# Optimization experiments

Hardware: AMD Instinct MI355X
Metric: run time of the kernel (lower is better)

## Reference

```python
import jax, jax.numpy as jnp
import numpy as np


def squash(s, axis=-1):
    sq = jnp.sum(s ** 2, axis=axis, keepdims=True)
    return sq / (1.0 + sq) * s / (jnp.sqrt(sq) + 1e-08)


def setup_inputs() -> dict:
    key = jax.random.key(0)
    B, C, H, W, D = 16, 64, 64, 64, 16
    inp = jax.random.normal(key, (B, C, H, W, D), dtype=jnp.float32)
    return {"inp": inp, "kernel_size": 2, "routing_iteration": 3}


def reference(inp, kernel_size, routing_iteration):
    B, C, H, W, D = inp.shape
    k = kernel_size
    nH, nW = H // k, W // k
    T = nH * nW
    kk = k * k
    # Extract non-overlapping k x k tiles (x-major, then y), flatten tile -> [B,C,T,kk,D]
    u = inp.reshape(B, C, nH, k, nW, k, D)
    u = u.transpose(0, 1, 2, 4, 3, 5, 6).reshape(B, C, T, kk, D)
    # u_hat gets a singleton "output capsule" axis (dim=1 in the original per-tile view)
    u_hat = u[:, :, :, None, :, :]            # [B,C,T,1,kk,D]
    temp_u_hat = jax.lax.stop_gradient(u_hat)  # detach
    b = jnp.zeros((B, C, T, 1, kk, 1), dtype=inp.dtype)
    for _ in range(routing_iteration - 1):
        c = jax.nn.softmax(b, axis=3)          # softmax over singleton axis -> ones (faithful)
        s = jnp.sum(c * temp_u_hat, axis=4)    # [B,C,T,1,D]
        v = squash(s)
        # uv = temp_u_hat @ v^T over D: [B,C,T,1,kk,1]
        uv = jnp.einsum('bctikd,bctid->bctik', temp_u_hat, v)[..., None]
        b = b + uv
    c = jax.nn.softmax(b, axis=3)
    s = jnp.sum(c * u_hat, axis=4)             # [B,C,T,1,D]
    v = squash(s)                              # [B,C,T,1,D]
    out = v[:, :, :, 0, :].reshape(B, C, nH, nW, D)
    return out
```

## Files before the change

### kernel.cpp

```cpp
#include <hip/hip_runtime.h>


#define B_  16
#define C_  64
#define H_  64
#define W_  64
#define D_  16
#define NH_ 32
#define NW_ 32
#define NVEC (B_ * C_ * NH_ * NW_)

typedef float f4 __attribute__((ext_vector_type(4)));

__global__ __launch_bounds__(256)
void caps_pool_squash_kernel(const float* __restrict__ in, float* __restrict__ out) {
    const unsigned stride = gridDim.x * 256u;
    const unsigned total  = NVEC * 4u;

    for (unsigned tid = blockIdx.x * 256u + threadIdx.x; tid < total; tid += stride) {
        const unsigned vec = tid >> 2;
        const unsigned q   = tid & 3u;

        const unsigned bc  = vec >> 10;
        const unsigned rem = vec & 1023u;
        const unsigned nh  = rem >> 5;
        const unsigned nw  = rem & 31u;

        const unsigned base = ((bc * H_ + 2u * nh) * W_ + 2u * nw) * D_ + q * 4u;

        const f4 a = __builtin_nontemporal_load((const f4*)(in + base));
        const f4 b = __builtin_nontemporal_load((const f4*)(in + base + D_));
        const f4 c = __builtin_nontemporal_load((const f4*)(in + base + W_ * D_));
        const f4 d = __builtin_nontemporal_load((const f4*)(in + base + W_ * D_ + D_));

        const f4 s = (a + b) + (c + d);

        float p = s.x * s.x + s.y * s.y + s.z * s.z + s.w * s.w;
        p += __shfl_xor(p, 1, 64);
        p += __shfl_xor(p, 2, 64);

        const float scale = p / ((1.0f + p) * (sqrtf(p) + 1e-8f));

        const f4 v = s * scale;
        __builtin_nontemporal_store(v, (f4*)(out + vec * (unsigned)D_ + q * 4u));
    }
}

extern "C" void kernel_launch(void* const* d_in, const int* in_sizes, int n_in,
                              void* d_out, int out_size, void* d_ws, size_t ws_size,
                              hipStream_t stream) {
    const float* inp = (const float*)d_in[0];
    float* out = (float*)d_out;

    caps_pool_squash_kernel<<<2048, 256, 0, stream>>>(inp, out);
}
```

Baseline: 62.55 us.

## Load contiguous rows per wave and pool 2x2 tiles via cross-lane shuffles

Each wavefront now handles 16 output capsules. It loads two full contiguous 1 KB input rows with one fully coalesced f4 per lane per segment, instead of four strided 64-byte pieces per capsule. The horizontal pair sum and the gather into output order are done with xor and indexed shuffles. The grid-stride loop is replaced by one launch covering all work exactly once, and the nontemporal load and store hints are dropped. This aims at better memory coalescing on a bandwidth-bound kernel, at the cost of extra shuffle instructions and possible cache pollution without the streaming hints.

```diff
diff --git a/kernel.cpp b/kernel.cpp
--- a/kernel.cpp
+++ b/kernel.cpp
@@ -6,44 +6,56 @@
 #define H_  64
 #define W_  64
 #define D_  16
-#define NH_ 32
-#define NW_ 32
-#define NVEC (B_ * C_ * NH_ * NW_)
+#define NVEC (B_ * C_ * 32 * 32)
 
 typedef float f4 __attribute__((ext_vector_type(4)));
 
 __global__ __launch_bounds__(256)
 void caps_pool_squash_kernel(const float* __restrict__ in, float* __restrict__ out) {
-    const unsigned stride = gridDim.x * 256u;
-    const unsigned total  = NVEC * 4u;
+    const unsigned tid  = blockIdx.x * 256u + threadIdx.x;
+    const unsigned wave = tid >> 6;
+    const unsigned lane = tid & 63u;
 
-    for (unsigned tid = blockIdx.x * 256u + threadIdx.x; tid < total; tid += stride) {
-        const unsigned vec = tid >> 2;
-        const unsigned q   = tid & 3u;
+    const unsigned bc  = wave >> 6;
+    const unsigned rem = (wave << 4) & 1023u;
+    const unsigned nh  = rem >> 5;
+    const unsigned nw0 = rem & 31u;
 
-        const unsigned bc  = vec >> 10;
-        const unsigned rem = vec & 1023u;
-        const unsigned nh  = rem >> 5;
-        const unsigned nw  = rem & 31u;
+    const unsigned ibase = bc * (H_ * W_ * D_) + (2u * nh) * (W_ * D_) + (2u * nw0) * D_;
 
-        const unsigned base = ((bc * H_ + 2u * nh) * W_ + 2u * nw) * D_ + q * 4u;
+    const f4 x0 = *(const f4*)(in + ibase + lane * 4u);
+    const f4 x1 = *(const f4*)(in + ibase + 256u + lane * 4u);
+    const f4 y0 = *(const f4*)(in + ibase + 1024u + lane * 4u);
+    const f4 y1 = *(const f4*)(in + ibase + 1280u + lane * 4u);
 
-        const f4 a = __builtin_nontemporal_load((const f4*)(in + base));
-        const f4 b = __builtin_nontemporal_load((const f4*)(in + base + D_));
-        const f4 c = __builtin_nontemporal_load((const f4*)(in + base + W_ * D_));
-        const f4 d = __builtin_nontemporal_load((const f4*)(in + base + W_ * D_ + D_));
+    f4 z0 = x0 + y0;
+    f4 z1 = x1 + y1;
 
-        const f4 s = (a + b) + (c + d);
+    z0.x += __shfl_xor(z0.x, 4, 64);  z0.y += __shfl_xor(z0.y, 4, 64);
+    z0.z += __shfl_xor(z0.z, 4, 64);  z0.w += __shfl_xor(z0.w, 4, 64);
+    z1.x += __shfl_xor(z1.x, 4, 64);  z1.y += __shfl_xor(z1.y, 4, 64);
+    z1.z += __shfl_xor(z1.z, 4, 64);  z1.w += __shfl_xor(z1.w, 4, 64);
 
-        float p = s.x * s.x + s.y * s.y + s.z * s.z + s.w * s.w;
-        p += __shfl_xor(p, 1, 64);
-        p += __shfl_xor(p, 2, 64);
+    const int src = (int)(((lane >> 2) & 7u) * 8u + (lane & 3u));
+    f4 s;
+    {
+        const float a0 = __shfl(z0.x, src, 64), b0 = __shfl(z1.x, src, 64);
+        const float a1 = __shfl(z0.y, src, 64), b1 = __shfl(z1.y, src, 64);
+        const float a2 = __shfl(z0.z, src, 64), b2 = __shfl(z1.z, src, 64);
+        const float a3 = __shfl(z0.w, src, 64), b3 = __shfl(z1.w, src, 64);
+        const bool lo = lane < 32u;
+        s.x = lo ? a0 : b0;  s.y = lo ? a1 : b1;
+        s.z = lo ? a2 : b2;  s.w = lo ? a3 : b3;
+    }
 
-        const float scale = p / ((1.0f + p) * (sqrtf(p) + 1e-8f));
+    float p = s.x * s.x + s.y * s.y + s.z * s.z + s.w * s.w;
+    p += __shfl_xor(p, 1, 64);
+    p += __shfl_xor(p, 2, 64);
+    const float scale = p / ((1.0f + p) * (sqrtf(p) + 1e-8f));
 
-        const f4 v = s * scale;
-        __builtin_nontemporal_store(v, (f4*)(out + vec * (unsigned)D_ + q * 4u));
-    }
+    const f4 v = s * scale;
+
+    *(f4*)(out + wave * 256u + lane * 4u) = v;
 }
 
 extern "C" void kernel_launch(void* const* d_in, const int* in_sizes, int n_in,
@@ -52,5 +64,7 @@
     const float* inp = (const float*)d_in[0];
     float* out = (float*)d_out;
 
-    caps_pool_squash_kernel<<<2048, 256, 0, stream>>>(inp, out);
+    const unsigned waves  = NVEC / 16u;
+    const unsigned blocks = (waves * 64u) / 256u;
+    caps_pool_squash_kernel<<<blocks, 256, 0, stream>>>(inp, out);
 }
```

Result: faster. 61.21 us (-2.1%).
